# Performance work log

Hardware: AMD Instinct MI355X
Metric: run time of the kernel (lower is better)

Reference implementation:

```python
import jax, jax.numpy as jnp
import numpy as np

HID = 1024
INTER = 4096
NUM_EXPERTS = 4096
NUM_KEYS = 64  # floor(sqrt(4096))
TOP_K = 8
B, S = 2, 2048


def setup_inputs() -> dict:
    key = jax.random.key(0)
    ks = jax.random.split(key, 7)
    sc = 0.02
    return {
        "hidden_states": jax.random.normal(ks[0], (B, S, HID), jnp.float32),
        "w_gate": jax.random.normal(ks[1], (INTER, HID), jnp.float32) * sc,
        "w_up": jax.random.normal(ks[2], (INTER, HID), jnp.float32) * sc,
        "w_down": jax.random.normal(ks[3], (HID, INTER), jnp.float32) * sc,
        "w_router": jax.random.normal(ks[4], (NUM_KEYS * 2, HID), jnp.float32) * sc,
        "down_embed": jax.random.normal(ks[5], (NUM_EXPERTS, HID), jnp.float32) * sc,
        "up_embed": jax.random.normal(ks[6], (NUM_EXPERTS, HID), jnp.float32) * sc,
    }


def reference(hidden_states, w_gate, w_up, w_down, w_router, down_embed, up_embed):
    b, s, h = hidden_states.shape
    n = b * s
    # router: [b,s,2*nk] -> row-major reshape to (2, n, nk), matching torch .view
    router_logits = (hidden_states @ w_router.T).reshape(2, n, NUM_KEYS)
    # topk with k == nk is a full descending sort (faithful to torch .topk)
    scores_xy, idx_xy = jax.lax.top_k(router_logits, NUM_KEYS)
    scores_x, scores_y = scores_xy[0], scores_xy[1]  # (n, nk) each
    idx_x, idx_y = idx_xy[0], idx_xy[1]
    all_scores = (scores_x[:, :, None] + scores_y[:, None, :]).reshape(n, NUM_KEYS * NUM_KEYS)
    all_indices = (idx_x[:, :, None] * NUM_KEYS + idx_y[:, None, :]).reshape(n, NUM_KEYS * NUM_KEYS)
    scores, pos = jax.lax.top_k(all_scores, TOP_K)  # (n, top_k)
    indices = jnp.take_along_axis(all_indices, pos, axis=-1)
    routing_weights = jax.nn.softmax(scores, axis=-1)
    routing_weights = routing_weights / routing_weights.sum(-1, keepdims=True)  # norm_topk_prob
    de = down_embed[indices]  # (n, top_k, h)
    ue = up_embed[indices]    # (n, top_k, h)
    x_flat = hidden_states.reshape(n, h)
    ew = jnp.einsum('nkh,nh->nk', de, x_flat)
    ew = jax.nn.silu(ew) * routing_weights
    experts_states = jnp.einsum('nk,nkh->nh', ew, ue).reshape(b, s, h)
    mlp = (jax.nn.silu(x_flat @ w_gate.T) * (x_flat @ w_up.T)) @ w_down.T
    out = mlp.reshape(b, s, h) + experts_states
    return (out, router_logits)
```

## Files before the change

kernel.cpp:

```cpp
#include <hip/hip_runtime.h>
#include <hip/hip_bf16.h>
#include <stdint.h>

typedef __bf16 bf16;
typedef __attribute__((ext_vector_type(8))) __bf16 bf16x8;
typedef __attribute__((ext_vector_type(4))) float f32x4;

static constexpr int kTok = 4096;
static constexpr int kHid = 1024;
static constexpr int kInter = 4096;

#define GLDS16(g, l)                                                \
  __builtin_amdgcn_global_load_lds(                                 \
      (const __attribute__((address_space(1))) void*)(g),           \
      (__attribute__((address_space(3))) void*)(l), 16, 0, 0)

__global__ void __launch_bounds__(256) k_cvt_rt(
    const float* X, const float* Wg, const float* Wu, const float* Wd,
    const float* Wr, bf16* Xb, bf16* Wgb, bf16* Wub, bf16* Wdb, float* out1) {
  __shared__ bf16 smem[8192];
  const int bid = blockIdx.x;
  const int t = threadIdx.x;

  if (bid < 32) {
    const int w = t >> 6;
    const int L = t & 63;
    const int la = L & 15;
    const int lk = (L >> 4) * 8;
    bf16* sA = smem;
    bf16* sB = smem + 4096;
    const long m0 = (long)bid * 128;
    const int wm = (w >> 1) * 64;
    const int wn = (w & 1) * 64;
    const f32x4 fzero = {0.f, 0.f, 0.f, 0.f};
    f32x4 acc[4][4];
#pragma unroll
    for (int i = 0; i < 4; ++i)
#pragma unroll
      for (int j = 0; j < 4; ++j) acc[i][j] = fzero;

    const int c0 = t, c1 = t + 256;
    const long ar0 = m0 + (c0 >> 2), ar1 = m0 + (c1 >> 2);
    const long br0 = (c0 >> 2), br1 = (c1 >> 2);
    const int ko = (c0 & 3) * 8;
    const bf16* sAr = sA + (wm + la) * 32 + lk;
    const bf16* sBr = sB + (wn + la) * 32 + lk;

    for (int kt = 0; kt < 32; ++kt) {
      const long k0 = (long)kt << 5;
      bf16x8 av0, av1, bv0, bv1;
      {
        const f32x4 x0 = *(const f32x4*)(X + ar0 * kHid + k0 + ko);
        const f32x4 x1 = *(const f32x4*)(X + ar0 * kHid + k0 + ko + 4);
        const f32x4 y0 = *(const f32x4*)(X + ar1 * kHid + k0 + ko);
        const f32x4 y1 = *(const f32x4*)(X + ar1 * kHid + k0 + ko + 4);
        const f32x4 p0 = *(const f32x4*)(Wr + br0 * kHid + k0 + ko);
        const f32x4 p1 = *(const f32x4*)(Wr + br0 * kHid + k0 + ko + 4);
        const f32x4 q0 = *(const f32x4*)(Wr + br1 * kHid + k0 + ko);
        const f32x4 q1 = *(const f32x4*)(Wr + br1 * kHid + k0 + ko + 4);
#pragma unroll
        for (int i = 0; i < 4; ++i) {
          av0[i] = (bf16)x0[i]; av0[4 + i] = (bf16)x1[i];
          av1[i] = (bf16)y0[i]; av1[4 + i] = (bf16)y1[i];
          bv0[i] = (bf16)p0[i]; bv0[4 + i] = (bf16)p1[i];
          bv1[i] = (bf16)q0[i]; bv1[4 + i] = (bf16)q1[i];
        }
      }
      __syncthreads();
      *(bf16x8*)(sA + c0 * 8) = av0;
      *(bf16x8*)(sA + c1 * 8) = av1;
      *(bf16x8*)(sB + c0 * 8) = bv0;
      *(bf16x8*)(sB + c1 * 8) = bv1;
      __syncthreads();
      bf16x8 af[4], bfm[4];
#pragma unroll
      for (int i = 0; i < 4; ++i) {
        af[i] = *(const bf16x8*)(sAr + i * 512);
        bfm[i] = *(const bf16x8*)(sBr + i * 512);
      }
#pragma unroll
      for (int i = 0; i < 4; ++i)
#pragma unroll
        for (int j = 0; j < 4; ++j)
          acc[i][j] = __builtin_amdgcn_mfma_f32_16x16x32_bf16(
              af[i], bfm[j], acc[i][j], 0, 0, 0);
    }
    const long col0 = wn + la;
    const long row0 = m0 + wm + (L >> 4) * 4;
#pragma unroll
    for (int i = 0; i < 4; ++i)
#pragma unroll
      for (int j = 0; j < 4; ++j)
#pragma unroll
        for (int r = 0; r < 4; ++r)
          out1[(row0 + i * 16 + r) * 128 + col0 + j * 16] = acc[i][j][r];
    return;
  }

  const int c = bid - 32;
  const float* src;
  bf16* dst;
  switch (c >> 11) {
    case 0: src = X;  dst = Xb;  break;
    case 1: src = Wg; dst = Wgb; break;
    case 2: src = Wu; dst = Wub; break;
    default: src = Wd; dst = Wdb; break;
  }
  const long i = ((long)(c & 2047) * 256 + t) * 8;
  const f32x4 a = *(const f32x4*)(src + i);
  const f32x4 b = *(const f32x4*)(src + i + 4);
  bf16x8 o;
#pragma unroll
  for (int k = 0; k < 4; ++k) { o[k] = (bf16)a[k]; o[4 + k] = (bf16)b[k]; }
  *(bf16x8*)(dst + i) = o;
}

__global__ void __launch_bounds__(256, 2) gemm_gu(
    const bf16* X, const bf16* Wg, const bf16* Wu, bf16* H) {
  constexpr int K = kHid, N = kInter;
  __shared__ bf16 sX[128 * 32];
  __shared__ bf16 sG[128 * 32];
  __shared__ bf16 sU[128 * 32];
  const int t = threadIdx.x;
  const int w = t >> 6;
  const int L = t & 63;
  const long m0 = (long)blockIdx.y * 128;
  const long n0 = (long)blockIdx.x * 128;
  const int wm = (w >> 1) * 64;
  const int wn = (w & 1) * 64;

  f32x4 accG[4][4], accU[4][4];
  const f32x4 fzero = {0.f, 0.f, 0.f, 0.f};
#pragma unroll
  for (int i = 0; i < 4; ++i)
#pragma unroll
    for (int j = 0; j < 4; ++j) { accG[i][j] = fzero; accU[i][j] = fzero; }

  const int r0 = t >> 2;
  const int ko = (t & 3) * 8;
  const bf16* gX0 = X + (m0 + r0) * K + ko;
  const bf16* gX1 = gX0 + (long)64 * K;
  const bf16* gG0 = Wg + (n0 + r0) * K + ko;
  const bf16* gG1 = gG0 + (long)64 * K;
  const bf16* gU0 = Wu + (n0 + r0) * K + ko;
  const bf16* gU1 = gU0 + (long)64 * K;
  bf16* lX0 = sX + w * 512;
  bf16* lX1 = sX + 2048 + w * 512;
  bf16* lG0 = sG + w * 512;
  bf16* lG1 = sG + 2048 + w * 512;
  bf16* lU0 = sU + w * 512;
  bf16* lU1 = sU + 2048 + w * 512;

  const int la = L & 15;
  const int lk = (L >> 4) * 8;
  const bf16* sXr = sX + (wm + la) * 32 + lk;
  const bf16* sGr = sG + (wn + la) * 32 + lk;
  const bf16* sUr = sU + (wn + la) * 32 + lk;

  for (int kt = 0; kt < K / 32; ++kt) {
    const long k0 = (long)kt << 5;
    GLDS16(gX0 + k0, lX0);
    GLDS16(gX1 + k0, lX1);
    GLDS16(gG0 + k0, lG0);
    GLDS16(gG1 + k0, lG1);
    GLDS16(gU0 + k0, lU0);
    GLDS16(gU1 + k0, lU1);
    __syncthreads();
    bf16x8 af[4], bg[4], bu[4];
#pragma unroll
    for (int i = 0; i < 4; ++i) {
      af[i] = *(const bf16x8*)(sXr + i * 512);
      bg[i] = *(const bf16x8*)(sGr + i * 512);
      bu[i] = *(const bf16x8*)(sUr + i * 512);
    }
#pragma unroll
    for (int i = 0; i < 4; ++i)
#pragma unroll
      for (int j = 0; j < 4; ++j) {
        accG[i][j] = __builtin_amdgcn_mfma_f32_16x16x32_bf16(af[i], bg[j],
                                                             accG[i][j], 0, 0, 0);
        accU[i][j] = __builtin_amdgcn_mfma_f32_16x16x32_bf16(af[i], bu[j],
                                                             accU[i][j], 0, 0, 0);
      }
    __syncthreads();
  }
  const long col0 = n0 + wn + la;
  const long row0 = m0 + wm + (L >> 4) * 4;
#pragma unroll
  for (int i = 0; i < 4; ++i)
#pragma unroll
    for (int j = 0; j < 4; ++j)
#pragma unroll
      for (int r = 0; r < 4; ++r) {
        const float g = accG[i][j][r];
        const float u = accU[i][j][r];
        H[(row0 + i * 16 + r) * N + col0 + j * 16] =
            (bf16)(g / (1.f + __expf(-g)) * u);
      }
}

__global__ void __launch_bounds__(256, 2) gemm_down(
    const bf16* Hs, const bf16* Wd, float* out0, float* p1) {
  constexpr int K = kInter, N = kHid;
  __shared__ bf16 sA[128 * 32];
  __shared__ bf16 sB[128 * 32];
  const int t = threadIdx.x;
  const int w = t >> 6;
  const int L = t & 63;
  const long m0 = (long)blockIdx.y * 128;
  const long n0 = (long)blockIdx.x * 128;
  const long zb = (long)blockIdx.z * 2048;
  const int wm = (w >> 1) * 64;
  const int wn = (w & 1) * 64;

  f32x4 acc[4][4];
  const f32x4 fzero = {0.f, 0.f, 0.f, 0.f};
#pragma unroll
  for (int i = 0; i < 4; ++i)
#pragma unroll
    for (int j = 0; j < 4; ++j) acc[i][j] = fzero;

  const int r0 = t >> 2;
  const int ko = (t & 3) * 8;
  const bf16* gA0 = Hs + (m0 + r0) * K + zb + ko;
  const bf16* gA1 = gA0 + (long)64 * K;
  const bf16* gB0 = Wd + (n0 + r0) * K + zb + ko;
  const bf16* gB1 = gB0 + (long)64 * K;
  bf16* lA0 = sA + w * 512;
  bf16* lA1 = sA + 2048 + w * 512;
  bf16* lB0 = sB + w * 512;
  bf16* lB1 = sB + 2048 + w * 512;

  const int la = L & 15;
  const int lk = (L >> 4) * 8;
  const bf16* sAr = sA + (wm + la) * 32 + lk;
  const bf16* sBr = sB + (wn + la) * 32 + lk;

  for (int kt = 0; kt < 64; ++kt) {
    const long k0 = (long)kt << 5;
    GLDS16(gA0 + k0, lA0);
    GLDS16(gA1 + k0, lA1);
    GLDS16(gB0 + k0, lB0);
    GLDS16(gB1 + k0, lB1);
    __syncthreads();
    bf16x8 af[4], bfm[4];
#pragma unroll
    for (int i = 0; i < 4; ++i) {
      af[i] = *(const bf16x8*)(sAr + i * 512);
      bfm[i] = *(const bf16x8*)(sBr + i * 512);
    }
#pragma unroll
    for (int i = 0; i < 4; ++i)
#pragma unroll
      for (int j = 0; j < 4; ++j)
        acc[i][j] = __builtin_amdgcn_mfma_f32_16x16x32_bf16(af[i], bfm[j],
                                                            acc[i][j], 0, 0, 0);
    __syncthreads();
  }
  float* dst = (blockIdx.z == 0) ? out0 : p1;
  const long col0 = n0 + wn + la;
  const long row0 = m0 + wm + (L >> 4) * 4;
#pragma unroll
  for (int i = 0; i < 4; ++i)
#pragma unroll
    for (int j = 0; j < 4; ++j)
#pragma unroll
      for (int r = 0; r < 4; ++r)
        dst[(row0 + i * 16 + r) * N + col0 + j * 16] = acc[i][j][r];
}

__global__ void __launch_bounds__(256) route_expert(
    const float* logits, const float* X, const float* dE, const float* uE,
    const float* p1, float* out0) {
  __shared__ float s_vals[4][128];
  __shared__ int s_idx[4][128];
  const int w = threadIdx.x >> 6;
  const int L = threadIdx.x & 63;
  const int j = blockIdx.x * 4 + w;

  const int half = (j & 1) * 64;
  const int rx = j >> 1;
  const float vx = logits[(long)rx * 128 + half + L];
  const float vy = logits[(long)(2048 + rx) * 128 + half + L];

  int rkx = 0, rky = 0;
  for (int m = 0; m < 64; ++m) {
    const float mx = __shfl(vx, m);
    const float my = __shfl(vy, m);
    rkx += (mx > vx) || (mx == vx && m < L);
    rky += (my > vy) || (my == vy && m < L);
  }
  rkx &= 63;
  rky &= 63;
  s_vals[w][rkx] = vx;
  s_idx[w][rkx] = L;
  s_vals[w][64 + rky] = vy;
  s_idx[w][64 + rky] = L;
  __syncthreads();

  int p = 0, q = 0;
  const bool valid = (L < 20);
  if (L < 8)       { p = L;      q = 0; }
  else if (L < 12) { p = L - 8;  q = 1; }
  else if (L < 14) { p = L - 12; q = 2; }
  else if (L < 16) { p = L - 14; q = 3; }
  else if (L < 20) { p = 0;      q = L - 12; }
  const float kNegBig = -3.0e38f;
  float myv = valid ? (s_vals[w][p] + s_vals[w][64 + q]) : kNegBig;
  int mypos = valid ? (p * 64 + q) : 0x7fffffff;

  float topv[8];
  int tope[8];
#pragma unroll
  for (int r = 0; r < 8; ++r) {
    float bv = myv;
    int bp = mypos;
#pragma unroll
    for (int d = 32; d > 0; d >>= 1) {
      const float ov = __shfl_xor(bv, d);
      const int op = __shfl_xor(bp, d);
      if (ov > bv || (ov == bv && op < bp)) { bv = ov; bp = op; }
    }
    topv[r] = bv;
    const int pp = (bp >> 6) & 127, qq = bp & 63;
    tope[r] = (s_idx[w][pp] * 64 + s_idx[w][64 + qq]) & 4095;
    if (mypos == bp) myv = kNegBig;
  }

  float e[8], wsum = 0.f;
#pragma unroll
  for (int r = 0; r < 8; ++r) {
    e[r] = __expf(topv[r] - topv[0]);
    wsum += e[r];
  }
  const float winv = 1.f / wsum;

  const long xoff = (long)j * kHid + L * 16;
  float xv[16], acc[16];
#pragma unroll
  for (int v4 = 0; v4 < 4; ++v4) {
    const f32x4 xl = *(const f32x4*)(X + xoff + v4 * 4);
#pragma unroll
    for (int i = 0; i < 4; ++i) { xv[v4 * 4 + i] = xl[i]; acc[v4 * 4 + i] = 0.f; }
  }

  for (int r = 0; r < 8; ++r) {
    const long eo = (long)tope[r] * kHid + L * 16;
    float d = 0.f;
#pragma unroll
    for (int v4 = 0; v4 < 4; ++v4) {
      const f32x4 dl = *(const f32x4*)(dE + eo + v4 * 4);
#pragma unroll
      for (int i = 0; i < 4; ++i) d += dl[i] * xv[v4 * 4 + i];
    }
#pragma unroll
    for (int dd = 32; dd > 0; dd >>= 1) d += __shfl_xor(d, dd);
    const float ew = d / (1.f + __expf(-d)) * (e[r] * winv);
#pragma unroll
    for (int v4 = 0; v4 < 4; ++v4) {
      const f32x4 ul = *(const f32x4*)(uE + eo + v4 * 4);
#pragma unroll
      for (int i = 0; i < 4; ++i) acc[v4 * 4 + i] += ew * ul[i];
    }
  }

  float* po = out0 + xoff;
  const float* pp1 = p1 + xoff;
#pragma unroll
  for (int v4 = 0; v4 < 4; ++v4) {
    f32x4 ov = *(const f32x4*)(po + v4 * 4);
    const f32x4 pv = *(const f32x4*)(pp1 + v4 * 4);
#pragma unroll
    for (int i = 0; i < 4; ++i) ov[i] += pv[i] + acc[v4 * 4 + i];
    *(f32x4*)(po + v4 * 4) = ov;
  }
}

extern "C" void kernel_launch(void* const* d_in, const int* in_sizes, int n_in,
                              void* d_out, int out_size, void* d_ws,
                              size_t ws_size, hipStream_t stream) {
  (void)in_sizes; (void)n_in; (void)out_size; (void)ws_size;
  const float* X  = (const float*)d_in[0];
  const float* Wg = (const float*)d_in[1];
  const float* Wu = (const float*)d_in[2];
  const float* Wd = (const float*)d_in[3];
  const float* Wr = (const float*)d_in[4];
  const float* dE = (const float*)d_in[5];
  const float* uE = (const float*)d_in[6];

  float* out0 = (float*)d_out;
  float* out1 = out0 + (size_t)kTok * kHid;

  bf16* wsH = (bf16*)d_ws;
  bf16* Xb  = wsH + (size_t)kTok * kInter;
  bf16* Wgb = Xb  + (size_t)kTok * kHid;
  bf16* Wub = Wgb + (size_t)kInter * kHid;
  bf16* Wdb = Wub + (size_t)kInter * kHid;
  float* p1 = (float*)Xb;

  dim3 blk(256);
  k_cvt_rt<<<dim3(8224), blk, 0, stream>>>(X, Wg, Wu, Wd, Wr,
                                           Xb, Wgb, Wub, Wdb, out1);
  gemm_gu<<<dim3(32, 32), blk, 0, stream>>>(Xb, Wgb, Wub, wsH);
  gemm_down<<<dim3(8, 32, 2), blk, 0, stream>>>(wsH, Wdb, out0, p1);
  route_expert<<<dim3(kTok / 4), blk, 0, stream>>>(out1, X, dE, uE, p1, out0);
}
```

Baseline: 371.5 us.

## Split each token's expert gather across four waves with LDS reduction

The route_expert kernel now assigns one token per block instead of one per wave. Each of the four waves handles two of the eight selected experts, issuing all down/up embedding loads up front, and the partial outputs are summed through shared memory by wave 0. This is meant to expose more memory-level parallelism in the latency-bound gather phase. The cost is that the routing/top-k computation is duplicated in all four waves and an extra LDS reduction and barrier are added.

```diff
diff --git a/kernel.cpp b/kernel.cpp
--- a/kernel.cpp
+++ b/kernel.cpp
@@ -270,13 +270,15 @@
 }
 
 __global__ void __launch_bounds__(256) route_expert(
-    const float* logits, const float* X, const float* dE, const float* uE,
-    const float* p1, float* out0) {
-  __shared__ float s_vals[4][128];
-  __shared__ int s_idx[4][128];
+    const float* __restrict__ logits, const float* __restrict__ X,
+    const float* __restrict__ dE, const float* __restrict__ uE,
+    const float* __restrict__ p1, float* __restrict__ out0) {
+  __shared__ float s_vals[128];
+  __shared__ int s_idx[128];
+  __shared__ float s_acc[3][16][64];
   const int w = threadIdx.x >> 6;
   const int L = threadIdx.x & 63;
-  const int j = blockIdx.x * 4 + w;
+  const int j = blockIdx.x;
 
   const int half = (j & 1) * 64;
   const int rx = j >> 1;
@@ -292,10 +294,10 @@
   }
   rkx &= 63;
   rky &= 63;
-  s_vals[w][rkx] = vx;
-  s_idx[w][rkx] = L;
-  s_vals[w][64 + rky] = vy;
-  s_idx[w][64 + rky] = L;
+  s_vals[rkx] = vx;
+  s_idx[rkx] = L;
+  s_vals[64 + rky] = vy;
+  s_idx[64 + rky] = L;
   __syncthreads();
 
   int p = 0, q = 0;
@@ -306,7 +308,7 @@
   else if (L < 16) { p = L - 14; q = 3; }
   else if (L < 20) { p = 0;      q = L - 12; }
   const float kNegBig = -3.0e38f;
-  float myv = valid ? (s_vals[w][p] + s_vals[w][64 + q]) : kNegBig;
+  float myv = valid ? (s_vals[p] + s_vals[64 + q]) : kNegBig;
   int mypos = valid ? (p * 64 + q) : 0x7fffffff;
 
   float topv[8];
@@ -323,7 +325,7 @@
     }
     topv[r] = bv;
     const int pp = (bp >> 6) & 127, qq = bp & 63;
-    tope[r] = (s_idx[w][pp] * 64 + s_idx[w][64 + qq]) & 4095;
+    tope[r] = (s_idx[pp] * 64 + s_idx[64 + qq]) & 4095;
     if (mypos == bp) myv = kNegBig;
   }
 
@@ -344,35 +346,68 @@
     for (int i = 0; i < 4; ++i) { xv[v4 * 4 + i] = xl[i]; acc[v4 * 4 + i] = 0.f; }
   }
 
-  for (int r = 0; r < 8; ++r) {
-    const long eo = (long)tope[r] * kHid + L * 16;
-    float d = 0.f;
+  const long lo16 = (long)L * 16;
+  const long eoA = (long)tope[2 * w] * kHid + lo16;
+  const long eoB = (long)tope[2 * w + 1] * kHid + lo16;
+  const f32x4 dA0 = *(const f32x4*)(dE + eoA);
+  const f32x4 dA1 = *(const f32x4*)(dE + eoA + 4);
+  const f32x4 dA2 = *(const f32x4*)(dE + eoA + 8);
+  const f32x4 dA3 = *(const f32x4*)(dE + eoA + 12);
+  const f32x4 dB0 = *(const f32x4*)(dE + eoB);
+  const f32x4 dB1 = *(const f32x4*)(dE + eoB + 4);
+  const f32x4 dB2 = *(const f32x4*)(dE + eoB + 8);
+  const f32x4 dB3 = *(const f32x4*)(dE + eoB + 12);
+  const f32x4 uA0 = *(const f32x4*)(uE + eoA);
+  const f32x4 uA1 = *(const f32x4*)(uE + eoA + 4);
+  const f32x4 uA2 = *(const f32x4*)(uE + eoA + 8);
+  const f32x4 uA3 = *(const f32x4*)(uE + eoA + 12);
+  const f32x4 uB0 = *(const f32x4*)(uE + eoB);
+  const f32x4 uB1 = *(const f32x4*)(uE + eoB + 4);
+  const f32x4 uB2 = *(const f32x4*)(uE + eoB + 8);
+  const f32x4 uB3 = *(const f32x4*)(uE + eoB + 12);
+
+  float da = 0.f, db = 0.f;
+#pragma unroll
+  for (int i = 0; i < 4; ++i) {
+    da += dA0[i] * xv[i] + dA1[i] * xv[4 + i] + dA2[i] * xv[8 + i] +
+          dA3[i] * xv[12 + i];
+    db += dB0[i] * xv[i] + dB1[i] * xv[4 + i] + dB2[i] * xv[8 + i] +
+          dB3[i] * xv[12 + i];
+  }
+#pragma unroll
+  for (int dd = 32; dd > 0; dd >>= 1) {
+    da += __shfl_xor(da, dd);
+    db += __shfl_xor(db, dd);
+  }
+  const float ewA = da / (1.f + __expf(-da)) * (e[2 * w] * winv);
+  const float ewB = db / (1.f + __expf(-db)) * (e[2 * w + 1] * winv);
+#pragma unroll
+  for (int i = 0; i < 4; ++i) {
+    acc[i]      += ewA * uA0[i] + ewB * uB0[i];
+    acc[4 + i]  += ewA * uA1[i] + ewB * uB1[i];
+    acc[8 + i]  += ewA * uA2[i] + ewB * uB2[i];
+    acc[12 + i] += ewA * uA3[i] + ewB * uB3[i];
+  }
+
+  if (w > 0) {
+#pragma unroll
+    for (int k = 0; k < 16; ++k) s_acc[w - 1][k][L] = acc[k];
+  }
+  __syncthreads();
+  if (w == 0) {
+#pragma unroll
+    for (int k = 0; k < 16; ++k)
+      acc[k] += s_acc[0][k][L] + s_acc[1][k][L] + s_acc[2][k][L];
+    float* po = out0 + xoff;
+    const float* pp1 = p1 + xoff;
 #pragma unroll
     for (int v4 = 0; v4 < 4; ++v4) {
-      const f32x4 dl = *(const f32x4*)(dE + eo + v4 * 4);
-#pragma unroll
-      for (int i = 0; i < 4; ++i) d += dl[i] * xv[v4 * 4 + i];
+      f32x4 ov = *(const f32x4*)(po + v4 * 4);
+      const f32x4 pv = *(const f32x4*)(pp1 + v4 * 4);
+#pragma unroll
+      for (int i = 0; i < 4; ++i) ov[i] += pv[i] + acc[v4 * 4 + i];
+      *(f32x4*)(po + v4 * 4) = ov;
     }
-#pragma unroll
-    for (int dd = 32; dd > 0; dd >>= 1) d += __shfl_xor(d, dd);
-    const float ew = d / (1.f + __expf(-d)) * (e[r] * winv);
-#pragma unroll
-    for (int v4 = 0; v4 < 4; ++v4) {
-      const f32x4 ul = *(const f32x4*)(uE + eo + v4 * 4);
-#pragma unroll
-      for (int i = 0; i < 4; ++i) acc[v4 * 4 + i] += ew * ul[i];
-    }
-  }
-
-  float* po = out0 + xoff;
-  const float* pp1 = p1 + xoff;
-#pragma unroll
-  for (int v4 = 0; v4 < 4; ++v4) {
-    f32x4 ov = *(const f32x4*)(po + v4 * 4);
-    const f32x4 pv = *(const f32x4*)(pp1 + v4 * 4);
-#pragma unroll
-    for (int i = 0; i < 4; ++i) ov[i] += pv[i] + acc[v4 * 4 + i];
-    *(f32x4*)(po + v4 * 4) = ov;
   }
 }
 
@@ -403,5 +438,5 @@
                                            Xb, Wgb, Wub, Wdb, out1);
   gemm_gu<<<dim3(32, 32), blk, 0, stream>>>(Xb, Wgb, Wub, wsH);
   gemm_down<<<dim3(8, 32, 2), blk, 0, stream>>>(wsH, Wdb, out0, p1);
-  route_expert<<<dim3(kTok / 4), blk, 0, stream>>>(out1, X, dE, uE, p1, out0);
+  route_expert<<<dim3(kTok), blk, 0, stream>>>(out1, X, dE, uE, p1, out0);
 }
```

After: 348.8 us. -6.1%, faster.
